# Optimization experiments

Measured on AMD Instinct MI355X. Metric: run time of the kernel, lower is better.

The kernel has to match this reference:

```python
import jax, jax.numpy as jnp
import numpy as np

B, T, D = 2, 2048, 2048
F = 2048          # hidden_dim // mp_size
E = 8             # num_experts (== num_local_experts, ep_size=1)
K = 2             # top_k


def setup_inputs() -> dict:
    key = jax.random.key(0)
    ks = jax.random.split(key, 6)
    s = 0.02
    return {
        "x": jax.random.normal(ks[0], (B, T, D), dtype=jnp.float32),
        "router_DE": jax.random.normal(ks[1], (D, E), dtype=jnp.float32) * s,
        "shared_w13": jax.random.normal(ks[2], (2 * F, D), dtype=jnp.float32) * s,
        "shared_w2": jax.random.normal(ks[3], (D, F), dtype=jnp.float32) * s,
        "routed_w13": jax.random.normal(ks[4], (E, 2 * F, D), dtype=jnp.float32) * s,
        "routed_w2": jax.random.normal(ks[5], (E, D, F), dtype=jnp.float32) * s,
        "use_static_shape": 1,
    }


def _swiglu(y):
    y0, y1 = jnp.split(y, 2, axis=-1)
    return y0 * jax.nn.sigmoid(y0) * y1


def reference(x, router_DE, shared_w13, shared_w2, routed_w13, routed_w2, use_static_shape):
    Bx, Tx, Dx = x.shape
    Tt = Bx * Tx
    tokens = x.reshape(Tt, Dx)                                   # (T, D)

    # Shared expert: SwiGLU MLP
    shared_y = tokens @ shared_w13.T                             # (T, 2F)
    shared_z = _swiglu(shared_y) @ shared_w2.T                   # (T, D)

    # Router: sigmoid scores + top-k
    scores = jax.nn.sigmoid(tokens @ router_DE)                  # (T, E)
    topk_values, topk_indices = jax.lax.top_k(scores, K)         # (T, K)

    # Scatter top-k gate values back into dense (T, E) mask
    rows = jnp.arange(Tt)[:, None]
    masked_scores = jnp.zeros_like(scores).at[rows, topk_indices].set(topk_values)

    # Dense baseline: gate tokens per expert, then per-expert SwiGLU MLP
    masked_tokens = masked_scores.T[:, :, None] * tokens[None]   # (E, T, D)
    h = jnp.einsum("etd,efd->etf", masked_tokens, routed_w13)    # (E, T, 2F)
    act = _swiglu(h)                                             # (E, T, F)
    z = jnp.einsum("etf,edf->etd", act, routed_w2)               # (E, T, D)

    out = z.sum(axis=0) + shared_z                               # (T, D)
    return out.reshape(Bx, Tx, Dx)
```

## Files before the change

kernel.cpp:

```cpp
#include <hip/hip_runtime.h>
#include <hip/hip_fp16.h>
#include <stdint.h>

#define TT 4096
#define DD 2048
#define FF 2048
#define EE 8
#define BM 128
#define BK 32
#define MAXPAD 9216

typedef _Float16 half8 __attribute__((ext_vector_type(8)));
typedef float f32x4 __attribute__((ext_vector_type(4)));

__device__ inline void gld_lds16(const _Float16* g, _Float16* l) {
    __builtin_amdgcn_global_load_lds(
        (const __attribute__((address_space(1))) uint32_t*)g,
        (__attribute__((address_space(3))) uint32_t*)l, 16, 0, 0);
}



__global__ void zero_cnt_kernel(int* cnt) {
    if (threadIdx.x < EE) cnt[threadIdx.x] = 0;
}

__global__ void cvt_f32_f16_kernel(const float* __restrict__ src,
                                   _Float16* __restrict__ dst, int n) {
    int i = (blockIdx.x * blockDim.x + threadIdx.x) * 4;
    if (i >= n) return;
    float4 v = *(const float4*)(src + i);
    union { _Float16 h[4]; uint2 u; } p;
    p.h[0] = (_Float16)v.x; p.h[1] = (_Float16)v.y;
    p.h[2] = (_Float16)v.z; p.h[3] = (_Float16)v.w;
    *(uint2*)(dst + i) = p.u;
}

__global__ void router_topk_kernel(const float* __restrict__ x,
                                   const float* __restrict__ rDE,
                                   int* __restrict__ cnt,
                                   int* __restrict__ tok_list,
                                   float* __restrict__ gate_list) {
    int t = blockIdx.x;
    __shared__ float red[256 * EE];
    float part[EE];
#pragma unroll
    for (int e = 0; e < EE; e++) part[e] = 0.f;
    const float* xr = x + (size_t)t * DD;
    for (int d = threadIdx.x; d < DD; d += 256) {
        float xv = xr[d];
        const float* rr = rDE + (size_t)d * EE;
#pragma unroll
        for (int e = 0; e < EE; e++) part[e] += xv * rr[e];
    }
#pragma unroll
    for (int e = 0; e < EE; e++) red[threadIdx.x * EE + e] = part[e];
    __syncthreads();
    for (int s = 128; s > 0; s >>= 1) {
        if (threadIdx.x < s) {
#pragma unroll
            for (int e = 0; e < EE; e++)
                red[threadIdx.x * EE + e] += red[(threadIdx.x + s) * EE + e];
        }
        __syncthreads();
    }
    if (threadIdx.x == 0) {
        float sc[EE];
#pragma unroll
        for (int e = 0; e < EE; e++) sc[e] = 1.f / (1.f + expf(-red[e]));
        int i0 = 0;
        for (int e = 1; e < EE; e++) if (sc[e] > sc[i0]) i0 = e;
        int i1 = -1;
        for (int e = 0; e < EE; e++) {
            if (e == i0) continue;
            if (i1 < 0 || sc[e] > sc[i1]) i1 = e;
        }
        int p0 = atomicAdd(&cnt[i0], 1);
        tok_list[i0 * TT + p0] = t; gate_list[i0 * TT + p0] = sc[i0];
        int p1 = atomicAdd(&cnt[i1], 1);
        tok_list[i1 * TT + p1] = t; gate_list[i1 * TT + p1] = sc[i1];
    }
}

__global__ void scan_offsets_kernel(const int* __restrict__ cnt, int* __restrict__ poff) {
    if (threadIdx.x == 0) {
        int off = 0;
        for (int e = 0; e < EE; e++) {
            poff[e] = off;
            off += ((cnt[e] + 127) >> 7) << 7;
        }
        poff[EE] = off;
    }
}

__global__ void gather_rows_kernel(const float* __restrict__ x,
                                   const int* __restrict__ cnt,
                                   const int* __restrict__ poff,
                                   const int* __restrict__ tok_list,
                                   const float* __restrict__ gate_list,
                                   _Float16* __restrict__ gath,
                                   int* __restrict__ rowinfo) {
    int b = blockIdx.x;
    if (b >= poff[EE]) return;
    int e = 0;
    while (b >= poff[e + 1]) e++;
    int i = b - poff[e];
    _Float16* dst = gath + (size_t)b * DD;
    if (i < cnt[e]) {
        int t = tok_list[e * TT + i];
        float g = gate_list[e * TT + i];
        if (threadIdx.x == 0) rowinfo[b] = t;
        const float* src = x + (size_t)t * DD;
        for (int d = threadIdx.x * 4; d < DD; d += 1024) {
            float4 v = *(const float4*)(src + d);
            union { _Float16 h[4]; uint2 u; } p;
            p.h[0] = (_Float16)(v.x * g); p.h[1] = (_Float16)(v.y * g);
            p.h[2] = (_Float16)(v.z * g); p.h[3] = (_Float16)(v.w * g);
            *(uint2*)(dst + d) = p.u;
        }
    } else {
        if (threadIdx.x == 0) rowinfo[b] = -1;
        uint2 z; z.x = 0u; z.y = 0u;
        for (int d = threadIdx.x * 4; d < DD; d += 1024)
            *(uint2*)(dst + d) = z;
    }
}


__global__ __launch_bounds__(256, 2)
void gemm_w13_swiglu_kernel(const _Float16* __restrict__ A,
                            const _Float16* __restrict__ W13,
                            _Float16* __restrict__ act,
                            const int* __restrict__ cnt,
                            const int* __restrict__ poff) {
    int row_base;
    const _Float16* w;
    if (cnt) {
        int e = blockIdx.z;
        int c = cnt[e];
        int mloc = blockIdx.y * BM;
        if (mloc >= c) return;
        row_base = poff[e] + mloc;
        w = W13 + (size_t)e * (2 * FF) * DD;
    } else {
        row_base = blockIdx.y * BM;
        w = W13;
    }
    int n_base = blockIdx.x * 128;

    __shared__ _Float16 lds[128 * BK * 3];

    const _Float16* srcA  = A + (size_t)row_base * DD;
    const _Float16* srcB0 = w + (size_t)n_base * DD;
    const _Float16* srcB1 = w + (size_t)(FF + n_base) * DD;

    int lane = threadIdx.x & 63;
    int wv = threadIdx.x >> 6;
    int wm = (wv >> 1) * 64;
    int wn = (wv & 1) * 64;
    int quad = lane >> 4;
    int l15 = lane & 15;
    int ldr = lane >> 2;
    int ldc = ((lane & 3) ^ ((lane >> 3) & 3)) * 8;
    int qx = (quad ^ ((l15 >> 1) & 3)) * 8;

    f32x4 acc0[4][4], acc1[4][4];
    f32x4 z4 = {0.f, 0.f, 0.f, 0.f};
#pragma unroll
    for (int m = 0; m < 4; m++)
#pragma unroll
        for (int n = 0; n < 4; n++) { acc0[m][n] = z4; acc1[m][n] = z4; }

    for (int kt = 0; kt < DD / BK; ++kt) {
        int k0 = kt * BK;
#pragma unroll
        for (int j = 0; j < 6; ++j) {
            int c = j * 4 + wv;
            int tile = c >> 3;
            int lc = c & 7;
            int r = lc * 16 + ldr;
            const _Float16* src = (tile == 0) ? srcA : (tile == 1) ? srcB0 : srcB1;
            gld_lds16(src + (size_t)r * DD + k0 + ldc, &lds[c * 512]);
        }
        __syncthreads();

        half8 a[4], b0[4], b1[4];
#pragma unroll
        for (int m = 0; m < 4; m++)
            a[m] = *(const half8*)(&lds[(wm + m * 16 + l15) * BK + qx]);
#pragma unroll
        for (int n = 0; n < 4; n++) {
            b0[n] = *(const half8*)(&lds[4096 + (wn + n * 16 + l15) * BK + qx]);
            b1[n] = *(const half8*)(&lds[8192 + (wn + n * 16 + l15) * BK + qx]);
        }
#pragma unroll
        for (int m = 0; m < 4; m++)
#pragma unroll
            for (int n = 0; n < 4; n++) {
                acc0[m][n] = __builtin_amdgcn_mfma_f32_16x16x32_f16(a[m], b0[n], acc0[m][n], 0, 0, 0);
                acc1[m][n] = __builtin_amdgcn_mfma_f32_16x16x32_f16(a[m], b1[n], acc1[m][n], 0, 0, 0);
            }
        __syncthreads();
    }

#pragma unroll
    for (int m = 0; m < 4; m++)
#pragma unroll
        for (int n = 0; n < 4; n++)
#pragma unroll
            for (int r = 0; r < 4; r++) {
                int row = row_base + wm + m * 16 + quad * 4 + r;
                int col = n_base + wn + n * 16 + l15;
                float y0 = acc0[m][n][r];
                float y1 = acc1[m][n][r];
                float v = y0 / (1.f + __expf(-y0)) * y1;
                act[(size_t)row * FF + col] = (_Float16)v;
            }
}

__global__ __launch_bounds__(256, 2)
void gemm_w2_kernel(const _Float16* __restrict__ Aact,
                    const _Float16* __restrict__ W2,
                    float* __restrict__ out,
                    const int* __restrict__ cnt,
                    const int* __restrict__ poff,
                    const int* __restrict__ rowinfo) {
    int row_base;
    const _Float16* w;
    if (cnt) {
        int e = blockIdx.z;
        int c = cnt[e];
        int mloc = blockIdx.y * BM;
        if (mloc >= c) return;
        row_base = poff[e] + mloc;
        w = W2 + (size_t)e * DD * FF;
    } else {
        row_base = blockIdx.y * BM;
        w = W2;
    }
    int n_base = blockIdx.x * 128;

    __shared__ _Float16 lds[128 * BK * 2];

    const _Float16* srcA = Aact + (size_t)row_base * FF;
    const _Float16* srcB = w + (size_t)n_base * FF;

    int lane = threadIdx.x & 63;
    int wv = threadIdx.x >> 6;
    int wm = (wv >> 1) * 64;
    int wn = (wv & 1) * 64;
    int quad = lane >> 4;
    int l15 = lane & 15;
    int ldr = lane >> 2;
    int ldc = ((lane & 3) ^ ((lane >> 3) & 3)) * 8;
    int qx = (quad ^ ((l15 >> 1) & 3)) * 8;

    f32x4 acc[4][4];
    f32x4 z4 = {0.f, 0.f, 0.f, 0.f};
#pragma unroll
    for (int m = 0; m < 4; m++)
#pragma unroll
        for (int n = 0; n < 4; n++) acc[m][n] = z4;

    for (int kt = 0; kt < FF / BK; ++kt) {
        int k0 = kt * BK;
#pragma unroll
        for (int j = 0; j < 4; ++j) {
            int c = j * 4 + wv;
            int tile = c >> 3;
            int lc = c & 7;
            int r = lc * 16 + ldr;
            const _Float16* src = (tile == 0) ? srcA : srcB;
            gld_lds16(src + (size_t)r * FF + k0 + ldc, &lds[c * 512]);
        }
        __syncthreads();

        half8 a[4], b[4];
#pragma unroll
        for (int m = 0; m < 4; m++)
            a[m] = *(const half8*)(&lds[(wm + m * 16 + l15) * BK + qx]);
#pragma unroll
        for (int n = 0; n < 4; n++)
            b[n] = *(const half8*)(&lds[4096 + (wn + n * 16 + l15) * BK + qx]);
#pragma unroll
        for (int m = 0; m < 4; m++)
#pragma unroll
            for (int n = 0; n < 4; n++)
                acc[m][n] = __builtin_amdgcn_mfma_f32_16x16x32_f16(a[m], b[n], acc[m][n], 0, 0, 0);
        __syncthreads();
    }

#pragma unroll
    for (int m = 0; m < 4; m++)
#pragma unroll
        for (int n = 0; n < 4; n++)
#pragma unroll
            for (int r = 0; r < 4; r++) {
                int row = row_base + wm + m * 16 + quad * 4 + r;
                int col = n_base + wn + n * 16 + l15;
                float v = acc[m][n][r];
                if (rowinfo) {
                    int t = rowinfo[row];
                    if (t >= 0) atomicAdd(&out[(size_t)t * DD + col], v);
                } else {
                    out[(size_t)row * DD + col] = v;
                }
            }
}


extern "C" void kernel_launch(void* const* d_in, const int* in_sizes, int n_in,
                              void* d_out, int out_size, void* d_ws, size_t ws_size,
                              hipStream_t stream) {
    const float* x     = (const float*)d_in[0];
    const float* rDE   = (const float*)d_in[1];
    const float* sw13  = (const float*)d_in[2];
    const float* sw2   = (const float*)d_in[3];
    const float* rw13  = (const float*)d_in[4];
    const float* rw2   = (const float*)d_in[5];
    float* out = (float*)d_out;

    char* ws = (char*)d_ws;
    size_t off = 0;
    auto alloc = [&](size_t bytes) {
        char* p = ws + off;
        off += (bytes + 255) & ~(size_t)255;
        return p;
    };
    _Float16* xh    = (_Float16*)alloc((size_t)TT * DD * 2);
    _Float16* sw13h = (_Float16*)alloc((size_t)2 * FF * DD * 2);
    _Float16* sw2h  = (_Float16*)alloc((size_t)DD * FF * 2);
    _Float16* rw13h = (_Float16*)alloc((size_t)EE * 2 * FF * DD * 2);
    _Float16* rw2h  = (_Float16*)alloc((size_t)EE * DD * FF * 2);
    _Float16* acts  = (_Float16*)alloc((size_t)TT * FF * 2);
    _Float16* gath  = (_Float16*)alloc((size_t)MAXPAD * DD * 2);
    _Float16* actr  = (_Float16*)alloc((size_t)MAXPAD * FF * 2);
    int* cnt        = (int*)alloc(EE * 4);
    int* poff       = (int*)alloc((EE + 1) * 4);
    int* tok_list   = (int*)alloc((size_t)EE * TT * 4);
    float* gate_list= (float*)alloc((size_t)EE * TT * 4);
    int* rowinfo    = (int*)alloc((size_t)MAXPAD * 4);

    zero_cnt_kernel<<<1, 64, 0, stream>>>(cnt);

    auto cvt = [&](const float* s, _Float16* d, int n) {
        cvt_f32_f16_kernel<<<(n / 4 + 255) / 256, 256, 0, stream>>>(s, d, n);
    };
    cvt(x,    xh,    TT * DD);
    cvt(sw13, sw13h, 2 * FF * DD);
    cvt(sw2,  sw2h,  DD * FF);
    cvt(rw13, rw13h, EE * 2 * FF * DD);
    cvt(rw2,  rw2h,  EE * DD * FF);

    router_topk_kernel<<<TT, 256, 0, stream>>>(x, rDE, cnt, tok_list, gate_list);
    scan_offsets_kernel<<<1, 64, 0, stream>>>(cnt, poff);
    gather_rows_kernel<<<MAXPAD, 256, 0, stream>>>(x, cnt, poff, tok_list, gate_list,
                                                   gath, rowinfo);

    gemm_w13_swiglu_kernel<<<dim3(FF / 128, TT / 128, 1), 256, 0, stream>>>(
        xh, sw13h, acts, nullptr, nullptr);
    gemm_w2_kernel<<<dim3(DD / 128, TT / 128, 1), 256, 0, stream>>>(
        acts, sw2h, out, nullptr, nullptr, nullptr);

    gemm_w13_swiglu_kernel<<<dim3(FF / 128, TT / 128, EE), 256, 0, stream>>>(
        gath, rw13h, actr, cnt, poff);
    gemm_w2_kernel<<<dim3(DD / 128, TT / 128, EE), 256, 0, stream>>>(
        actr, rw2h, out, cnt, poff, rowinfo);
}
```

Baseline: 1.170 ms.

## Double-buffer LDS tiles in expert GEMMs to overlap global loads with MFMA

Both grouped GEMM kernels (W13+SwiGLU and W2) now use two LDS slots. The next K-tile is issued with global_load_lds before computing on the current one, with a manual vmcnt wait and raw s_barrier in place of __syncthreads. s_setprio raises wave priority around the MFMA block. This aims to hide global-memory latency behind matrix math, at the cost of doubled LDS use, which may lower occupancy, and fragile hand-tuned waitcnt values.

```diff
diff --git a/kernel.cpp b/kernel.cpp
--- a/kernel.cpp
+++ b/kernel.cpp
@@ -148,7 +148,7 @@
     }
     int n_base = blockIdx.x * 128;
 
-    __shared__ _Float16 lds[128 * BK * 3];
+    __shared__ _Float16 lds[2 * 128 * BK * 3];
 
     const _Float16* srcA  = A + (size_t)row_base * DD;
     const _Float16* srcB0 = w + (size_t)n_base * DD;
@@ -171,8 +171,9 @@
 #pragma unroll
         for (int n = 0; n < 4; n++) { acc0[m][n] = z4; acc1[m][n] = z4; }
 
-    for (int kt = 0; kt < DD / BK; ++kt) {
+    auto stage = [&](int kt, int slot) {
         int k0 = kt * BK;
+        _Float16* dstb = &lds[slot * 12288];
 #pragma unroll
         for (int j = 0; j < 6; ++j) {
             int c = j * 4 + wv;
@@ -180,19 +181,34 @@
             int lc = c & 7;
             int r = lc * 16 + ldr;
             const _Float16* src = (tile == 0) ? srcA : (tile == 1) ? srcB0 : srcB1;
-            gld_lds16(src + (size_t)r * DD + k0 + ldc, &lds[c * 512]);
-        }
-        __syncthreads();
-
+            gld_lds16(src + (size_t)r * DD + k0 + ldc, dstb + c * 512);
+        }
+    };
+
+    constexpr int NT = DD / BK;
+    stage(0, 0);
+    for (int kt = 0; kt < NT; ++kt) {
+        int cur = kt & 1;
+        if (kt + 1 < NT) {
+            stage(kt + 1, cur ^ 1);
+            asm volatile("s_waitcnt vmcnt(6)" ::: "memory");
+        } else {
+            asm volatile("s_waitcnt vmcnt(0)" ::: "memory");
+        }
+        __builtin_amdgcn_s_barrier();
+        asm volatile("" ::: "memory");
+
+        const _Float16* lb = &lds[cur * 12288];
         half8 a[4], b0[4], b1[4];
 #pragma unroll
         for (int m = 0; m < 4; m++)
-            a[m] = *(const half8*)(&lds[(wm + m * 16 + l15) * BK + qx]);
+            a[m] = *(const half8*)(&lb[(wm + m * 16 + l15) * BK + qx]);
 #pragma unroll
         for (int n = 0; n < 4; n++) {
-            b0[n] = *(const half8*)(&lds[4096 + (wn + n * 16 + l15) * BK + qx]);
-            b1[n] = *(const half8*)(&lds[8192 + (wn + n * 16 + l15) * BK + qx]);
-        }
+            b0[n] = *(const half8*)(&lb[4096 + (wn + n * 16 + l15) * BK + qx]);
+            b1[n] = *(const half8*)(&lb[8192 + (wn + n * 16 + l15) * BK + qx]);
+        }
+        __builtin_amdgcn_s_setprio(1);
 #pragma unroll
         for (int m = 0; m < 4; m++)
 #pragma unroll
@@ -200,7 +216,10 @@
                 acc0[m][n] = __builtin_amdgcn_mfma_f32_16x16x32_f16(a[m], b0[n], acc0[m][n], 0, 0, 0);
                 acc1[m][n] = __builtin_amdgcn_mfma_f32_16x16x32_f16(a[m], b1[n], acc1[m][n], 0, 0, 0);
             }
-        __syncthreads();
+        __builtin_amdgcn_s_setprio(0);
+        asm volatile("" ::: "memory");
+        __builtin_amdgcn_s_barrier();
+        asm volatile("" ::: "memory");
     }
 
 #pragma unroll
@@ -240,7 +259,7 @@
     }
     int n_base = blockIdx.x * 128;
 
-    __shared__ _Float16 lds[128 * BK * 2];
+    __shared__ _Float16 lds[2 * 128 * BK * 2];
 
     const _Float16* srcA = Aact + (size_t)row_base * FF;
     const _Float16* srcB = w + (size_t)n_base * FF;
@@ -262,8 +281,9 @@
 #pragma unroll
         for (int n = 0; n < 4; n++) acc[m][n] = z4;
 
-    for (int kt = 0; kt < FF / BK; ++kt) {
+    auto stage = [&](int kt, int slot) {
         int k0 = kt * BK;
+        _Float16* dstb = &lds[slot * 8192];
 #pragma unroll
         for (int j = 0; j < 4; ++j) {
             int c = j * 4 + wv;
@@ -271,23 +291,41 @@
             int lc = c & 7;
             int r = lc * 16 + ldr;
             const _Float16* src = (tile == 0) ? srcA : srcB;
-            gld_lds16(src + (size_t)r * FF + k0 + ldc, &lds[c * 512]);
-        }
-        __syncthreads();
-
+            gld_lds16(src + (size_t)r * FF + k0 + ldc, dstb + c * 512);
+        }
+    };
+
+    constexpr int NT = FF / BK;
+    stage(0, 0);
+    for (int kt = 0; kt < NT; ++kt) {
+        int cur = kt & 1;
+        if (kt + 1 < NT) {
+            stage(kt + 1, cur ^ 1);
+            asm volatile("s_waitcnt vmcnt(4)" ::: "memory");
+        } else {
+            asm volatile("s_waitcnt vmcnt(0)" ::: "memory");
+        }
+        __builtin_amdgcn_s_barrier();
+        asm volatile("" ::: "memory");
+
+        const _Float16* lb = &lds[cur * 8192];
         half8 a[4], b[4];
 #pragma unroll
         for (int m = 0; m < 4; m++)
-            a[m] = *(const half8*)(&lds[(wm + m * 16 + l15) * BK + qx]);
+            a[m] = *(const half8*)(&lb[(wm + m * 16 + l15) * BK + qx]);
 #pragma unroll
         for (int n = 0; n < 4; n++)
-            b[n] = *(const half8*)(&lds[4096 + (wn + n * 16 + l15) * BK + qx]);
+            b[n] = *(const half8*)(&lb[4096 + (wn + n * 16 + l15) * BK + qx]);
+        __builtin_amdgcn_s_setprio(1);
 #pragma unroll
         for (int m = 0; m < 4; m++)
 #pragma unroll
             for (int n = 0; n < 4; n++)
                 acc[m][n] = __builtin_amdgcn_mfma_f32_16x16x32_f16(a[m], b[n], acc[m][n], 0, 0, 0);
-        __syncthreads();
+        __builtin_amdgcn_s_setprio(0);
+        asm volatile("" ::: "memory");
+        __builtin_amdgcn_s_barrier();
+        asm volatile("" ::: "memory");
     }
 
 #pragma unroll
```

After: 1.593 ms. 1.36x slower.

## Split fused W13 SwiGLU GEMM into two half-width GEMM passes

Applied to the files above, without the earlier changes.

The fused gate/up GEMM, which kept two 128x128 accumulator sets per block, is replaced by a kernel that computes one half at a time. The first pass writes silu(gate) to the activation buffer and the second multiplies it by the up projection. This halves accumulator registers and LDS per block, which may allow higher occupancy. In exchange, the A tiles are loaded twice and the activation buffer makes an extra fp16 round trip through memory, and the extra silu rounding to fp16 costs a little precision.

```diff
diff --git a/kernel.cpp b/kernel.cpp
--- a/kernel.cpp
+++ b/kernel.cpp
@@ -128,11 +128,13 @@
 
 
 __global__ __launch_bounds__(256, 2)
-void gemm_w13_swiglu_kernel(const _Float16* __restrict__ A,
-                            const _Float16* __restrict__ W13,
-                            _Float16* __restrict__ act,
-                            const int* __restrict__ cnt,
-                            const int* __restrict__ poff) {
+void gemm_w13_half_kernel(const _Float16* __restrict__ A,
+                          const _Float16* __restrict__ W,
+                          _Float16* __restrict__ act,
+                          int mode,
+                          const int* __restrict__ cnt,
+                          const int* __restrict__ poff,
+                          size_t estride) {
     int row_base;
     const _Float16* w;
     if (cnt) {
@@ -141,18 +143,17 @@
         int mloc = blockIdx.y * BM;
         if (mloc >= c) return;
         row_base = poff[e] + mloc;
-        w = W13 + (size_t)e * (2 * FF) * DD;
+        w = W + (size_t)e * estride;
     } else {
         row_base = blockIdx.y * BM;
-        w = W13;
+        w = W;
     }
     int n_base = blockIdx.x * 128;
 
-    __shared__ _Float16 lds[128 * BK * 3];
-
-    const _Float16* srcA  = A + (size_t)row_base * DD;
-    const _Float16* srcB0 = w + (size_t)n_base * DD;
-    const _Float16* srcB1 = w + (size_t)(FF + n_base) * DD;
+    __shared__ _Float16 lds[128 * BK * 2];
+
+    const _Float16* srcA = A + (size_t)row_base * DD;
+    const _Float16* srcB = w + (size_t)n_base * DD;
 
     int lane = threadIdx.x & 63;
     int wv = threadIdx.x >> 6;
@@ -164,42 +165,38 @@
     int ldc = ((lane & 3) ^ ((lane >> 3) & 3)) * 8;
     int qx = (quad ^ ((l15 >> 1) & 3)) * 8;
 
-    f32x4 acc0[4][4], acc1[4][4];
+    f32x4 acc[4][4];
     f32x4 z4 = {0.f, 0.f, 0.f, 0.f};
 #pragma unroll
     for (int m = 0; m < 4; m++)
 #pragma unroll
-        for (int n = 0; n < 4; n++) { acc0[m][n] = z4; acc1[m][n] = z4; }
+        for (int n = 0; n < 4; n++) acc[m][n] = z4;
 
     for (int kt = 0; kt < DD / BK; ++kt) {
         int k0 = kt * BK;
 #pragma unroll
-        for (int j = 0; j < 6; ++j) {
+        for (int j = 0; j < 4; ++j) {
             int c = j * 4 + wv;
             int tile = c >> 3;
             int lc = c & 7;
             int r = lc * 16 + ldr;
-            const _Float16* src = (tile == 0) ? srcA : (tile == 1) ? srcB0 : srcB1;
+            const _Float16* src = (tile == 0) ? srcA : srcB;
             gld_lds16(src + (size_t)r * DD + k0 + ldc, &lds[c * 512]);
         }
         __syncthreads();
 
-        half8 a[4], b0[4], b1[4];
+        half8 a[4], b[4];
 #pragma unroll
         for (int m = 0; m < 4; m++)
             a[m] = *(const half8*)(&lds[(wm + m * 16 + l15) * BK + qx]);
 #pragma unroll
-        for (int n = 0; n < 4; n++) {
-            b0[n] = *(const half8*)(&lds[4096 + (wn + n * 16 + l15) * BK + qx]);
-            b1[n] = *(const half8*)(&lds[8192 + (wn + n * 16 + l15) * BK + qx]);
-        }
+        for (int n = 0; n < 4; n++)
+            b[n] = *(const half8*)(&lds[4096 + (wn + n * 16 + l15) * BK + qx]);
 #pragma unroll
         for (int m = 0; m < 4; m++)
 #pragma unroll
-            for (int n = 0; n < 4; n++) {
-                acc0[m][n] = __builtin_amdgcn_mfma_f32_16x16x32_f16(a[m], b0[n], acc0[m][n], 0, 0, 0);
-                acc1[m][n] = __builtin_amdgcn_mfma_f32_16x16x32_f16(a[m], b1[n], acc1[m][n], 0, 0, 0);
-            }
+            for (int n = 0; n < 4; n++)
+                acc[m][n] = __builtin_amdgcn_mfma_f32_16x16x32_f16(a[m], b[n], acc[m][n], 0, 0, 0);
         __syncthreads();
     }
 
@@ -211,10 +208,14 @@
             for (int r = 0; r < 4; r++) {
                 int row = row_base + wm + m * 16 + quad * 4 + r;
                 int col = n_base + wn + n * 16 + l15;
-                float y0 = acc0[m][n][r];
-                float y1 = acc1[m][n][r];
-                float v = y0 / (1.f + __expf(-y0)) * y1;
-                act[(size_t)row * FF + col] = (_Float16)v;
+                size_t idx = (size_t)row * FF + col;
+                float v = acc[m][n][r];
+                if (mode == 0) {
+                    act[idx] = (_Float16)(v / (1.f + __expf(-v)));
+                } else {
+                    float t = (float)act[idx];
+                    act[idx] = (_Float16)(t * v);
+                }
             }
 }
 
@@ -357,13 +358,20 @@
     gather_rows_kernel<<<MAXPAD, 256, 0, stream>>>(x, cnt, poff, tok_list, gate_list,
                                                    gath, rowinfo);
 
-    gemm_w13_swiglu_kernel<<<dim3(FF / 128, TT / 128, 1), 256, 0, stream>>>(
-        xh, sw13h, acts, nullptr, nullptr);
+    const size_t w13_half_off = (size_t)FF * DD;
+    const size_t w13_estride  = (size_t)2 * FF * DD;
+
+    gemm_w13_half_kernel<<<dim3(FF / 128, TT / 128, 1), 256, 0, stream>>>(
+        xh, sw13h, acts, 0, nullptr, nullptr, 0);
+    gemm_w13_half_kernel<<<dim3(FF / 128, TT / 128, 1), 256, 0, stream>>>(
+        xh, sw13h + w13_half_off, acts, 1, nullptr, nullptr, 0);
     gemm_w2_kernel<<<dim3(DD / 128, TT / 128, 1), 256, 0, stream>>>(
         acts, sw2h, out, nullptr, nullptr, nullptr);
 
-    gemm_w13_swiglu_kernel<<<dim3(FF / 128, TT / 128, EE), 256, 0, stream>>>(
-        gath, rw13h, actr, cnt, poff);
+    gemm_w13_half_kernel<<<dim3(FF / 128, TT / 128, EE), 256, 0, stream>>>(
+        gath, rw13h, actr, 0, cnt, poff, w13_estride);
+    gemm_w13_half_kernel<<<dim3(FF / 128, TT / 128, EE), 256, 0, stream>>>(
+        gath, rw13h + w13_half_off, actr, 1, cnt, poff, w13_estride);
     gemm_w2_kernel<<<dim3(DD / 128, TT / 128, EE), 256, 0, stream>>>(
         actr, rw2h, out, cnt, poff, rowinfo);
 }
```

New measurement: 1.264 ms. 1.08x slower.

## Merge shared and routed GEMMs, widen tiles, replace atomics with combine pass

Applied to the files above, without the earlier changes.

Doubles the K tile to 64 and adopts an 8-way XOR swizzle for LDS. The shared and routed expert GEMMs now run in single launches by using an extra grid z slice, and the w2 GEMM uses a 128x256 output tile. Routed w2 results are written densely to a scratch buffer that aliases the gathered-input space, and a separate combine kernel, using per-token metadata recorded by the router, adds them into the output. This removes the float atomics and the fused launches, at the cost of more registers for the wider w2 tile and an extra pass over the output. The combine kernel depends on the shared w2 slice having finished, which holds because it is a later launch on the same stream.

```diff
diff --git a/kernel.cpp b/kernel.cpp
--- a/kernel.cpp
+++ b/kernel.cpp
@@ -7,7 +7,7 @@
 #define FF 2048
 #define EE 8
 #define BM 128
-#define BK 32
+#define BK 64
 #define MAXPAD 9216
 
 typedef _Float16 half8 __attribute__((ext_vector_type(8)));
@@ -40,7 +40,8 @@
                                    const float* __restrict__ rDE,
                                    int* __restrict__ cnt,
                                    int* __restrict__ tok_list,
-                                   float* __restrict__ gate_list) {
+                                   float* __restrict__ gate_list,
+                                   int4* __restrict__ meta) {
     int t = blockIdx.x;
     __shared__ float red[256 * EE];
     float part[EE];
@@ -79,6 +80,7 @@
         tok_list[i0 * TT + p0] = t; gate_list[i0 * TT + p0] = sc[i0];
         int p1 = atomicAdd(&cnt[i1], 1);
         tok_list[i1 * TT + p1] = t; gate_list[i1 * TT + p1] = sc[i1];
+        meta[t] = make_int4(i0, p0, i1, p1);
     }
 }
 
@@ -98,8 +100,7 @@
                                    const int* __restrict__ poff,
                                    const int* __restrict__ tok_list,
                                    const float* __restrict__ gate_list,
-                                   _Float16* __restrict__ gath,
-                                   int* __restrict__ rowinfo) {
+                                   _Float16* __restrict__ gath) {
     int b = blockIdx.x;
     if (b >= poff[EE]) return;
     int e = 0;
@@ -109,7 +110,6 @@
     if (i < cnt[e]) {
         int t = tok_list[e * TT + i];
         float g = gate_list[e * TT + i];
-        if (threadIdx.x == 0) rowinfo[b] = t;
         const float* src = x + (size_t)t * DD;
         for (int d = threadIdx.x * 4; d < DD; d += 1024) {
             float4 v = *(const float4*)(src + d);
@@ -119,7 +119,6 @@
             *(uint2*)(dst + d) = p.u;
         }
     } else {
-        if (threadIdx.x == 0) rowinfo[b] = -1;
         uint2 z; z.x = 0u; z.y = 0u;
         for (int d = threadIdx.x * 4; d < DD; d += 1024)
             *(uint2*)(dst + d) = z;
@@ -128,29 +127,34 @@
 
 
 __global__ __launch_bounds__(256, 2)
-void gemm_w13_swiglu_kernel(const _Float16* __restrict__ A,
-                            const _Float16* __restrict__ W13,
-                            _Float16* __restrict__ act,
-                            const int* __restrict__ cnt,
-                            const int* __restrict__ poff) {
-    int row_base;
-    const _Float16* w;
-    if (cnt) {
-        int e = blockIdx.z;
-        int c = cnt[e];
+void gemm_w13_kernel(const _Float16* __restrict__ xh,
+                     const _Float16* __restrict__ gath,
+                     const _Float16* __restrict__ sw13,
+                     const _Float16* __restrict__ rw13,
+                     _Float16* __restrict__ acts,
+                     _Float16* __restrict__ actr,
+                     const int* __restrict__ cnt,
+                     const int* __restrict__ poff) {
+    int z = blockIdx.z;
+    const _Float16 *srcA, *w;
+    _Float16* dst;
+    if (z == EE) {
+        srcA = xh + (size_t)blockIdx.y * BM * DD;
+        w = sw13;
+        dst = acts + (size_t)blockIdx.y * BM * FF;
+    } else {
+        int c = cnt[z];
         int mloc = blockIdx.y * BM;
         if (mloc >= c) return;
-        row_base = poff[e] + mloc;
-        w = W13 + (size_t)e * (2 * FF) * DD;
-    } else {
-        row_base = blockIdx.y * BM;
-        w = W13;
+        int rb = poff[z] + mloc;
+        srcA = gath + (size_t)rb * DD;
+        w = rw13 + (size_t)z * (2 * FF) * DD;
+        dst = actr + (size_t)rb * FF;
     }
     int n_base = blockIdx.x * 128;
 
-    __shared__ _Float16 lds[128 * BK * 3];
-
-    const _Float16* srcA  = A + (size_t)row_base * DD;
+    __shared__ _Float16 lds[3 * 128 * BK];
+
     const _Float16* srcB0 = w + (size_t)n_base * DD;
     const _Float16* srcB1 = w + (size_t)(FF + n_base) * DD;
 
@@ -160,9 +164,8 @@
     int wn = (wv & 1) * 64;
     int quad = lane >> 4;
     int l15 = lane & 15;
-    int ldr = lane >> 2;
-    int ldc = ((lane & 3) ^ ((lane >> 3) & 3)) * 8;
-    int qx = (quad ^ ((l15 >> 1) & 3)) * 8;
+    int srow = lane >> 3;
+    int sk = ((lane & 7) ^ srow) * 8;
 
     f32x4 acc0[4][4], acc1[4][4];
     f32x4 z4 = {0.f, 0.f, 0.f, 0.f};
@@ -174,32 +177,39 @@
     for (int kt = 0; kt < DD / BK; ++kt) {
         int k0 = kt * BK;
 #pragma unroll
-        for (int j = 0; j < 6; ++j) {
+        for (int j = 0; j < 12; ++j) {
             int c = j * 4 + wv;
-            int tile = c >> 3;
-            int lc = c & 7;
-            int r = lc * 16 + ldr;
+            int tile = c >> 4;
+            int lc = c & 15;
+            int r = lc * 8 + srow;
             const _Float16* src = (tile == 0) ? srcA : (tile == 1) ? srcB0 : srcB1;
-            gld_lds16(src + (size_t)r * DD + k0 + ldc, &lds[c * 512]);
+            gld_lds16(src + (size_t)r * DD + k0 + sk, &lds[c * 512]);
         }
         __syncthreads();
 
-        half8 a[4], b0[4], b1[4];
-#pragma unroll
-        for (int m = 0; m < 4; m++)
-            a[m] = *(const half8*)(&lds[(wm + m * 16 + l15) * BK + qx]);
-#pragma unroll
-        for (int n = 0; n < 4; n++) {
-            b0[n] = *(const half8*)(&lds[4096 + (wn + n * 16 + l15) * BK + qx]);
-            b1[n] = *(const half8*)(&lds[8192 + (wn + n * 16 + l15) * BK + qx]);
-        }
-#pragma unroll
-        for (int m = 0; m < 4; m++)
+#pragma unroll
+        for (int ks = 0; ks < 2; ++ks) {
+            half8 a[4], b0[4], b1[4];
+#pragma unroll
+            for (int m = 0; m < 4; m++) {
+                int ra = wm + m * 16 + l15;
+                a[m] = *(const half8*)(&lds[ra * BK + (((ks * 4 + quad) ^ (ra & 7)) * 8)]);
+            }
 #pragma unroll
             for (int n = 0; n < 4; n++) {
-                acc0[m][n] = __builtin_amdgcn_mfma_f32_16x16x32_f16(a[m], b0[n], acc0[m][n], 0, 0, 0);
-                acc1[m][n] = __builtin_amdgcn_mfma_f32_16x16x32_f16(a[m], b1[n], acc1[m][n], 0, 0, 0);
-            }
+                int rb = wn + n * 16 + l15;
+                int px = ((ks * 4 + quad) ^ (rb & 7)) * 8;
+                b0[n] = *(const half8*)(&lds[8192 + rb * BK + px]);
+                b1[n] = *(const half8*)(&lds[16384 + rb * BK + px]);
+            }
+#pragma unroll
+            for (int m = 0; m < 4; m++)
+#pragma unroll
+                for (int n = 0; n < 4; n++) {
+                    acc0[m][n] = __builtin_amdgcn_mfma_f32_16x16x32_f16(a[m], b0[n], acc0[m][n], 0, 0, 0);
+                    acc1[m][n] = __builtin_amdgcn_mfma_f32_16x16x32_f16(a[m], b1[n], acc1[m][n], 0, 0, 0);
+                }
+        }
         __syncthreads();
     }
 
@@ -209,103 +219,130 @@
         for (int n = 0; n < 4; n++)
 #pragma unroll
             for (int r = 0; r < 4; r++) {
-                int row = row_base + wm + m * 16 + quad * 4 + r;
+                int row = wm + m * 16 + quad * 4 + r;
                 int col = n_base + wn + n * 16 + l15;
                 float y0 = acc0[m][n][r];
                 float y1 = acc1[m][n][r];
                 float v = y0 / (1.f + __expf(-y0)) * y1;
-                act[(size_t)row * FF + col] = (_Float16)v;
+                dst[(size_t)row * FF + col] = (_Float16)v;
             }
 }
 
 __global__ __launch_bounds__(256, 2)
-void gemm_w2_kernel(const _Float16* __restrict__ Aact,
-                    const _Float16* __restrict__ W2,
+void gemm_w2_kernel(const _Float16* __restrict__ acts,
+                    const _Float16* __restrict__ actr,
+                    const _Float16* __restrict__ sw2,
+                    const _Float16* __restrict__ rw2,
                     float* __restrict__ out,
+                    float* __restrict__ zr,
                     const int* __restrict__ cnt,
-                    const int* __restrict__ poff,
-                    const int* __restrict__ rowinfo) {
-    int row_base;
-    const _Float16* w;
-    if (cnt) {
-        int e = blockIdx.z;
-        int c = cnt[e];
+                    const int* __restrict__ poff) {
+    int z = blockIdx.z;
+    const _Float16 *srcA, *w;
+    float* dst;
+    if (z == EE) {
+        srcA = acts + (size_t)blockIdx.y * BM * FF;
+        w = sw2;
+        dst = out + (size_t)blockIdx.y * BM * DD;
+    } else {
+        int c = cnt[z];
         int mloc = blockIdx.y * BM;
         if (mloc >= c) return;
-        row_base = poff[e] + mloc;
-        w = W2 + (size_t)e * DD * FF;
-    } else {
-        row_base = blockIdx.y * BM;
-        w = W2;
-    }
-    int n_base = blockIdx.x * 128;
-
-    __shared__ _Float16 lds[128 * BK * 2];
-
-    const _Float16* srcA = Aact + (size_t)row_base * FF;
+        int rb = poff[z] + mloc;
+        srcA = actr + (size_t)rb * FF;
+        w = rw2 + (size_t)z * DD * FF;
+        dst = zr + (size_t)rb * DD;
+    }
+    int n_base = blockIdx.x * 256;
+
+    __shared__ _Float16 lds[(128 + 256) * BK];
+
     const _Float16* srcB = w + (size_t)n_base * FF;
 
     int lane = threadIdx.x & 63;
     int wv = threadIdx.x >> 6;
     int wm = (wv >> 1) * 64;
-    int wn = (wv & 1) * 64;
+    int wn = (wv & 1) * 128;
     int quad = lane >> 4;
     int l15 = lane & 15;
-    int ldr = lane >> 2;
-    int ldc = ((lane & 3) ^ ((lane >> 3) & 3)) * 8;
-    int qx = (quad ^ ((l15 >> 1) & 3)) * 8;
-
-    f32x4 acc[4][4];
+    int srow = lane >> 3;
+    int sk = ((lane & 7) ^ srow) * 8;
+
+    f32x4 acc[4][8];
     f32x4 z4 = {0.f, 0.f, 0.f, 0.f};
 #pragma unroll
     for (int m = 0; m < 4; m++)
 #pragma unroll
-        for (int n = 0; n < 4; n++) acc[m][n] = z4;
+        for (int n = 0; n < 8; n++) acc[m][n] = z4;
 
     for (int kt = 0; kt < FF / BK; ++kt) {
         int k0 = kt * BK;
 #pragma unroll
-        for (int j = 0; j < 4; ++j) {
+        for (int j = 0; j < 12; ++j) {
             int c = j * 4 + wv;
-            int tile = c >> 3;
-            int lc = c & 7;
-            int r = lc * 16 + ldr;
-            const _Float16* src = (tile == 0) ? srcA : srcB;
-            gld_lds16(src + (size_t)r * FF + k0 + ldc, &lds[c * 512]);
+            const _Float16* src;
+            if (c < 16) {
+                int r = c * 8 + srow;
+                src = srcA + (size_t)r * FF + k0 + sk;
+            } else {
+                int r = (c - 16) * 8 + srow;
+                src = srcB + (size_t)r * FF + k0 + sk;
+            }
+            gld_lds16(src, &lds[c * 512]);
         }
         __syncthreads();
 
-        half8 a[4], b[4];
-#pragma unroll
-        for (int m = 0; m < 4; m++)
-            a[m] = *(const half8*)(&lds[(wm + m * 16 + l15) * BK + qx]);
-#pragma unroll
-        for (int n = 0; n < 4; n++)
-            b[n] = *(const half8*)(&lds[4096 + (wn + n * 16 + l15) * BK + qx]);
-#pragma unroll
-        for (int m = 0; m < 4; m++)
-#pragma unroll
-            for (int n = 0; n < 4; n++)
-                acc[m][n] = __builtin_amdgcn_mfma_f32_16x16x32_f16(a[m], b[n], acc[m][n], 0, 0, 0);
+#pragma unroll
+        for (int ks = 0; ks < 2; ++ks) {
+            half8 a[4], b[8];
+#pragma unroll
+            for (int m = 0; m < 4; m++) {
+                int ra = wm + m * 16 + l15;
+                a[m] = *(const half8*)(&lds[ra * BK + (((ks * 4 + quad) ^ (ra & 7)) * 8)]);
+            }
+#pragma unroll
+            for (int n = 0; n < 8; n++) {
+                int rb = wn + n * 16 + l15;
+                b[n] = *(const half8*)(&lds[8192 + rb * BK + (((ks * 4 + quad) ^ (rb & 7)) * 8)]);
+            }
+#pragma unroll
+            for (int m = 0; m < 4; m++)
+#pragma unroll
+                for (int n = 0; n < 8; n++)
+                    acc[m][n] = __builtin_amdgcn_mfma_f32_16x16x32_f16(a[m], b[n], acc[m][n], 0, 0, 0);
+        }
         __syncthreads();
     }
 
 #pragma unroll
     for (int m = 0; m < 4; m++)
 #pragma unroll
-        for (int n = 0; n < 4; n++)
+        for (int n = 0; n < 8; n++)
 #pragma unroll
             for (int r = 0; r < 4; r++) {
-                int row = row_base + wm + m * 16 + quad * 4 + r;
+                int row = wm + m * 16 + quad * 4 + r;
                 int col = n_base + wn + n * 16 + l15;
-                float v = acc[m][n][r];
-                if (rowinfo) {
-                    int t = rowinfo[row];
-                    if (t >= 0) atomicAdd(&out[(size_t)t * DD + col], v);
-                } else {
-                    out[(size_t)row * DD + col] = v;
-                }
-            }
+                dst[(size_t)row * DD + col] = acc[m][n][r];
+            }
+}
+
+__global__ void combine_kernel(const int4* __restrict__ meta,
+                               const int* __restrict__ poff,
+                               const float* __restrict__ zr,
+                               float* __restrict__ out) {
+    int t = blockIdx.x;
+    int4 m = meta[t];
+    const float* z0 = zr + (size_t)(poff[m.x] + m.y) * DD;
+    const float* z1 = zr + (size_t)(poff[m.z] + m.w) * DD;
+    float* o = out + (size_t)t * DD;
+    for (int d = threadIdx.x * 4; d < DD; d += 1024) {
+        float4 a = *(const float4*)(o + d);
+        float4 u = *(const float4*)(z0 + d);
+        float4 v = *(const float4*)(z1 + d);
+        a.x += u.x + v.x; a.y += u.y + v.y;
+        a.z += u.z + v.z; a.w += u.w + v.w;
+        *(float4*)(o + d) = a;
+    }
 }
 
 
@@ -333,13 +370,15 @@
     _Float16* rw13h = (_Float16*)alloc((size_t)EE * 2 * FF * DD * 2);
     _Float16* rw2h  = (_Float16*)alloc((size_t)EE * DD * FF * 2);
     _Float16* acts  = (_Float16*)alloc((size_t)TT * FF * 2);
-    _Float16* gath  = (_Float16*)alloc((size_t)MAXPAD * DD * 2);
     _Float16* actr  = (_Float16*)alloc((size_t)MAXPAD * FF * 2);
     int* cnt        = (int*)alloc(EE * 4);
     int* poff       = (int*)alloc((EE + 1) * 4);
     int* tok_list   = (int*)alloc((size_t)EE * TT * 4);
     float* gate_list= (float*)alloc((size_t)EE * TT * 4);
-    int* rowinfo    = (int*)alloc((size_t)MAXPAD * 4);
+    int4* meta      = (int4*)alloc((size_t)TT * 16);
+    _Float16* gath  = (_Float16*)alloc((size_t)MAXPAD * DD * 2);
+    alloc((size_t)MAXPAD * DD * 2);
+    float* zr = (float*)gath;
 
     zero_cnt_kernel<<<1, 64, 0, stream>>>(cnt);
 
@@ -352,18 +391,13 @@
     cvt(rw13, rw13h, EE * 2 * FF * DD);
     cvt(rw2,  rw2h,  EE * DD * FF);
 
-    router_topk_kernel<<<TT, 256, 0, stream>>>(x, rDE, cnt, tok_list, gate_list);
+    router_topk_kernel<<<TT, 256, 0, stream>>>(x, rDE, cnt, tok_list, gate_list, meta);
     scan_offsets_kernel<<<1, 64, 0, stream>>>(cnt, poff);
-    gather_rows_kernel<<<MAXPAD, 256, 0, stream>>>(x, cnt, poff, tok_list, gate_list,
-                                                   gath, rowinfo);
-
-    gemm_w13_swiglu_kernel<<<dim3(FF / 128, TT / 128, 1), 256, 0, stream>>>(
-        xh, sw13h, acts, nullptr, nullptr);
-    gemm_w2_kernel<<<dim3(DD / 128, TT / 128, 1), 256, 0, stream>>>(
-        acts, sw2h, out, nullptr, nullptr, nullptr);
-
-    gemm_w13_swiglu_kernel<<<dim3(FF / 128, TT / 128, EE), 256, 0, stream>>>(
-        gath, rw13h, actr, cnt, poff);
-    gemm_w2_kernel<<<dim3(DD / 128, TT / 128, EE), 256, 0, stream>>>(
-        actr, rw2h, out, cnt, poff, rowinfo);
-}
+    gather_rows_kernel<<<MAXPAD, 256, 0, stream>>>(x, cnt, poff, tok_list, gate_list, gath);
+
+    gemm_w13_kernel<<<dim3(FF / 128, TT / 128, EE + 1), 256, 0, stream>>>(
+        xh, gath, sw13h, rw13h, acts, actr, cnt, poff);
+    gemm_w2_kernel<<<dim3(DD / 256, TT / 128, EE + 1), 256, 0, stream>>>(
+        acts, actr, sw2h, rw2h, out, zr, cnt, poff);
+    combine_kernel<<<TT, 256, 0, stream>>>(meta, poff, zr, out);
+}
```

New measurement: 1.028 ms. 1.14x faster.
